# Kernel tuning notes

Measured on AMD Instinct MI355X. Metric: run time of the kernel, lower is better.

## Reference

```python
import jax, jax.numpy as jnp
import numpy as np

# opt constants baked from init_kwargs
OPT_M = 1024      # number of OFDM subcarriers (opt.M)
N_PILOT = 0       # opt.N_pilot
VELOCITY = 100.0  # opt.V (is_random_v=False)
DECAY = 4.0       # opt.decay
C_LIGHT = 3.0e8
CARRIER_FREQ = 3.0e9


def setup_inputs() -> dict:
    key = jax.random.key(0)
    k1, k2 = jax.random.split(key, 2)
    N, P, L, M, S = 16, 4, 16, OPT_M, 128
    # channel tap power profile: exp(-l/decay), normalized
    power = jnp.exp(-jnp.arange(L, dtype=jnp.float32) / DECAY)
    power = power / jnp.sum(power)
    # Rayleigh(sigma=1) samples = sqrt(g1^2 + g2^2), g_i ~ N(0,1)
    g = jax.random.normal(k1, (N, P, L, 2), dtype=jnp.float32)
    rayleigh = jnp.sqrt(g[..., 0] ** 2 + g[..., 1] ** 2)
    cof = jnp.sqrt(power / 2.0) * rayleigh  # (N,P,L), strictly positive
    input_ri = jax.random.normal(k2, (N, P, S * M, 2), dtype=jnp.float32)
    return {"input_ri": input_ri, "cof": cof, "Ns": 128}


def reference(input_ri, cof, Ns):
    N, P, SMK, _ = input_ri.shape
    L = cof.shape[-1]
    S = Ns + N_PILOT  # OFDM mode: S = Ns + N_pilot, M = opt.M
    Mk = SMK // S
    x = (input_ri[..., 0] + 1j * input_ri[..., 1]).astype(jnp.complex64)  # (N,P,SMK)

    # per-tap propagation delay from tap gain: len = -100*log(cof); delay1 = len/c
    delay1 = (-100.0 * jnp.log(cof)) / C_LIGHT                      # (N,P,L)
    delay2 = jnp.linspace(0.0, (S - 1) * (0.0005 / 14.0), S).astype(jnp.float32)  # (S,)
    delay = delay1[..., None] + delay2                              # (N,P,L,S)

    max_doppler = VELOCITY / C_LIGHT * CARRIER_FREQ
    angles = jnp.linspace(0.0, 2.0 * np.pi, L).astype(jnp.float32)  # (L,)
    phase_coef = (2.0 * np.pi * jnp.cos(angles) * max_doppler)      # (L,)
    phases = phase_coef[None, None, :, None] * delay                # (N,P,L,S)
    shift = jnp.exp(-1j * phases.astype(jnp.float32))               # complex64 (N,P,L,S)

    # sum over taps L BEFORE multiplying by the L-independent input (same math,
    # avoids materializing the (N,P,L,S,M) broadcast intermediate)
    factor = jnp.sum(cof[..., None].astype(jnp.complex64) * shift, axis=2)  # (N,P,S)
    out = x.reshape(N, P, S, Mk) * factor[..., None]                # (N,P,S,M)
    out = out.reshape(N, P, SMK)
    out_ri = jnp.stack([out.real, out.imag], axis=-1)               # (N,P,SMK,2)

    # frequency response H_t = FFT of zero-padded taps
    cof_zp = jnp.concatenate([cof, jnp.zeros((N, P, OPT_M - L), cof.dtype)], axis=-1)
    H_t = jnp.fft.fft(cof_zp.astype(jnp.complex64), axis=-1)        # (N,P,OPT_M)
    H_t_ri = jnp.stack([H_t.real, H_t.imag], axis=-1)
    return out_ri, H_t_ri
```

## Files before the change

### kernel.cpp

```cpp
#include <hip/hip_runtime.h>
#include <math.h>

#define NB     16
#define PB     4
#define LTAPS  16
#define SS     128
#define MM     1024

#define TWO_PI_F 6.28318530717958647692f

#define HT_BLKS     256
#define STREAM_BLKS 2048
#define TOT4 (NB * PB * SS * MM / 2)

typedef float f32x4 __attribute__((ext_vector_type(4)));

__global__ __launch_bounds__(256) void fused_kernel(
    const float* __restrict__ in,
    const float* __restrict__ cof,
    float* __restrict__ out,
    float* __restrict__ ht)
{
    const int b = blockIdx.x;
    const int t = threadIdx.x;

    if (b >= HT_BLKS) {
        const int sb = b - HT_BLKS;

        const f32x4* __restrict__ in4  = (const f32x4*)in + (size_t)sb * 2048;
        f32x4* __restrict__       out4 = (f32x4*)out      + (size_t)sb * 2048;
        f32x4 v[8];
#pragma unroll
        for (int k = 0; k < 8; ++k)
            v[k] = __builtin_nontemporal_load(&in4[k * 256 + t]);

        const int lane = t & 63;
        const int j    = lane >> 4;
        const int l    = lane & 15;
        const int id   = sb * 4 + j;
        const int np   = id >> 7;
        const int s    = id & (SS - 1);
        const float cofl   = cof[np * LTAPS + l];
        const float delay1 = (-100.0f / 3.0e8f) * logf(cofl);
        const float delay2 = (0.0005f / 14.0f) * (float)s;
        const float pc     = TWO_PI_F * 1000.0f * cosf((TWO_PI_F / 15.0f) * (float)l);
        const float ph     = pc * (delay1 + delay2);
        float sn, cs;
        sincosf(ph, &sn, &cs);
        float re = cofl * cs;
        float im = -cofl * sn;
#pragma unroll
        for (int w = 1; w < 16; w <<= 1) {
            re += __shfl_xor(re, w);
            im += __shfl_xor(im, w);
        }
        float fre[4], fim[4];
#pragma unroll
        for (int jj = 0; jj < 4; ++jj) {
            fre[jj] = __shfl(re, jj * 16);
            fim[jj] = __shfl(im, jj * 16);
        }

#pragma unroll
        for (int k = 0; k < 8; ++k) {
            const int jj = k >> 1;
            f32x4 r;
            r.x = v[k].x * fre[jj] - v[k].y * fim[jj];
            r.y = v[k].x * fim[jj] + v[k].y * fre[jj];
            r.z = v[k].z * fre[jj] - v[k].w * fim[jj];
            r.w = v[k].z * fim[jj] + v[k].w * fre[jj];
            __builtin_nontemporal_store(r, &out4[k * 256 + t]);
        }
    } else {
        const int id = b * 256 + t;
        const int np = id >> 10;
        const int k  = id & (MM - 1);
        float sn, cs;
        sincosf((TWO_PI_F / (float)MM) * (float)k, &sn, &cs);
        const float wr = cs, wi = -sn;
        const float* __restrict__ c = cof + np * LTAPS;
        float hr = 0.0f, hi = 0.0f;
        float cr = 1.0f, ci = 0.0f;
#pragma unroll
        for (int l = 0; l < LTAPS; ++l) {
            const float cl = c[l];
            hr += cl * cr;
            hi += cl * ci;
            const float nr = cr * wr - ci * wi;
            const float ni = cr * wi + ci * wr;
            cr = nr; ci = ni;
        }
        float2* __restrict__ o = (float2*)ht;
        o[id] = make_float2(hr, hi);
    }
}

extern "C" void kernel_launch(void* const* d_in, const int* in_sizes, int n_in,
                              void* d_out, int out_size, void* d_ws, size_t ws_size,
                              hipStream_t stream)
{
    const float* in  = (const float*)d_in[0];
    const float* cof = (const float*)d_in[1];
    float* out = (float*)d_out;
    float* ht  = out + (size_t)NB * PB * SS * MM * 2;

    hipLaunchKernelGGL(fused_kernel, dim3(HT_BLKS + STREAM_BLKS), dim3(256), 0, stream,
                       in, cof, out, ht);
}
```

Measured before the change: 25.63 us.

## Split streaming loads into two halves, use fast intrinsics, raise occupancy hint

The streaming path now issues the first four vector loads, computes the phase factor, then loads the second four, so fewer values need to be held in registers at once. Accurate logf/cosf/sincosf are replaced with the fast __logf/__cosf/__sincosf intrinsics in both paths to shorten the transcendental code. Launch bounds now request 8 blocks per CU. The risks are less memory-level parallelism per thread, because the second half of the loads no longer overlaps the factor computation, and lower accuracy for large phase arguments in the fast sincos.

```diff
diff --git a/kernel.cpp b/kernel.cpp
--- a/kernel.cpp
+++ b/kernel.cpp
@@ -15,7 +15,7 @@
 
 typedef float f32x4 __attribute__((ext_vector_type(4)));
 
-__global__ __launch_bounds__(256) void fused_kernel(
+__global__ __launch_bounds__(256, 8) void fused_kernel(
     const float* __restrict__ in,
     const float* __restrict__ cof,
     float* __restrict__ out,
@@ -26,13 +26,13 @@
 
     if (b >= HT_BLKS) {
         const int sb = b - HT_BLKS;
-
         const f32x4* __restrict__ in4  = (const f32x4*)in + (size_t)sb * 2048;
         f32x4* __restrict__       out4 = (f32x4*)out      + (size_t)sb * 2048;
-        f32x4 v[8];
+
+        f32x4 v0[4];
 #pragma unroll
-        for (int k = 0; k < 8; ++k)
-            v[k] = __builtin_nontemporal_load(&in4[k * 256 + t]);
+        for (int k = 0; k < 4; ++k)
+            v0[k] = __builtin_nontemporal_load(&in4[k * 256 + t]);
 
         const int lane = t & 63;
         const int j    = lane >> 4;
@@ -41,12 +41,12 @@
         const int np   = id >> 7;
         const int s    = id & (SS - 1);
         const float cofl   = cof[np * LTAPS + l];
-        const float delay1 = (-100.0f / 3.0e8f) * logf(cofl);
+        const float delay1 = (-100.0f / 3.0e8f) * __logf(cofl);
         const float delay2 = (0.0005f / 14.0f) * (float)s;
-        const float pc     = TWO_PI_F * 1000.0f * cosf((TWO_PI_F / 15.0f) * (float)l);
+        const float pc     = TWO_PI_F * 1000.0f * __cosf((TWO_PI_F / 15.0f) * (float)l);
         const float ph     = pc * (delay1 + delay2);
         float sn, cs;
-        sincosf(ph, &sn, &cs);
+        __sincosf(ph, &sn, &cs);
         float re = cofl * cs;
         float im = -cofl * sn;
 #pragma unroll
@@ -61,22 +61,37 @@
             fim[jj] = __shfl(im, jj * 16);
         }
 
+        f32x4 v1[4];
 #pragma unroll
-        for (int k = 0; k < 8; ++k) {
+        for (int k = 0; k < 4; ++k)
+            v1[k] = __builtin_nontemporal_load(&in4[(k + 4) * 256 + t]);
+
+#pragma unroll
+        for (int k = 0; k < 4; ++k) {
             const int jj = k >> 1;
             f32x4 r;
-            r.x = v[k].x * fre[jj] - v[k].y * fim[jj];
-            r.y = v[k].x * fim[jj] + v[k].y * fre[jj];
-            r.z = v[k].z * fre[jj] - v[k].w * fim[jj];
-            r.w = v[k].z * fim[jj] + v[k].w * fre[jj];
+            r.x = v0[k].x * fre[jj] - v0[k].y * fim[jj];
+            r.y = v0[k].x * fim[jj] + v0[k].y * fre[jj];
+            r.z = v0[k].z * fre[jj] - v0[k].w * fim[jj];
+            r.w = v0[k].z * fim[jj] + v0[k].w * fre[jj];
             __builtin_nontemporal_store(r, &out4[k * 256 + t]);
+        }
+#pragma unroll
+        for (int k = 0; k < 4; ++k) {
+            const int jj = (k + 4) >> 1;
+            f32x4 r;
+            r.x = v1[k].x * fre[jj] - v1[k].y * fim[jj];
+            r.y = v1[k].x * fim[jj] + v1[k].y * fre[jj];
+            r.z = v1[k].z * fre[jj] - v1[k].w * fim[jj];
+            r.w = v1[k].z * fim[jj] + v1[k].w * fre[jj];
+            __builtin_nontemporal_store(r, &out4[(k + 4) * 256 + t]);
         }
     } else {
         const int id = b * 256 + t;
         const int np = id >> 10;
         const int k  = id & (MM - 1);
         float sn, cs;
-        sincosf((TWO_PI_F / (float)MM) * (float)k, &sn, &cs);
+        __sincosf((TWO_PI_F / (float)MM) * (float)k, &sn, &cs);
         const float wr = cs, wi = -sn;
         const float* __restrict__ c = cof + np * LTAPS;
         float hr = 0.0f, hi = 0.0f;
```

Result: no change. 25.85 us (+0.9%).
